# Kernel optimization log

Hardware: AMD Instinct MI355X
Metric: run time of the kernel (lower is better)

## Reference

```python
import jax, jax.numpy as jnp
import numpy as np


def _set_abstraction(xyz, points, npoint, nsample, w1, b1, w2, b2, w3, b3):
    """xyz: (B,3,N), points: (B,C,N) or None. Returns (new_xyz, new_points).
    BN (eval mode) is folded into conv weights/biases; conv1x1 == einsum over channels.
    Deterministic sampling: take first `npoint` points (stand-in for randperm)."""
    B, _, N = xyz.shape
    if npoint is None:
        new_xyz = xyz
        P = N
    else:
        new_xyz = xyz[:, :, :npoint]
        P = npoint
    # squared pairwise distances (B,P,N); topk indices match cdist topk (sqrt monotone)
    xs = jnp.sum(new_xyz * new_xyz, axis=1)            # (B,P)
    ys = jnp.sum(xyz * xyz, axis=1)                    # (B,N)
    d2 = xs[:, :, None] + ys[:, None, :] - 2.0 * jnp.einsum('bcp,bcn->bpn', new_xyz, xyz)
    _, idx = jax.lax.top_k(-d2, nsample)               # (B,P,K) nearest neighbors
    idx4 = idx[:, None, :, :]                          # (B,1,P,K)
    grouped_xyz = jnp.take_along_axis(xyz[:, :, None, :], idx4, axis=3)  # (B,3,P,K)
    grouped_xyz = grouped_xyz - new_xyz[:, :, :, None]
    if points is not None:
        grouped_pts = jnp.take_along_axis(points[:, :, None, :], idx4, axis=3)  # (B,C,P,K)
        feat = jnp.concatenate([grouped_xyz, grouped_pts], axis=1)
    else:
        feat = grouped_xyz
    h = jax.nn.relu(jnp.einsum('oc,bcpk->bopk', w1, feat) + b1[None, :, None, None])
    h = jax.nn.relu(jnp.einsum('oc,bcpk->bopk', w2, h) + b2[None, :, None, None])
    h = jnp.einsum('oc,bcpk->bopk', w3, h) + b3[None, :, None, None]  # no relu before max
    new_points = jnp.max(h, axis=3)                    # (B,C_out,P) max over nsample
    return new_xyz, new_points


def setup_inputs() -> dict:
    key = jax.random.key(0)
    ks = iter(jax.random.split(key, 32))
    B, N, C_IN, NUM_CLASSES = 32, 4096, 6, 40

    def w(k, co, ci):
        return jax.random.normal(k, (co, ci), dtype=jnp.float32) * (1.0 / np.sqrt(ci))

    def b(k, co):
        return jax.random.normal(k, (co,), dtype=jnp.float32) * 0.01

    inp = {'x': jax.random.normal(next(ks), (B, C_IN, N), dtype=jnp.float32)}
    # sa1: in = 3 feat + 3 rel-xyz = 6
    inp['sa1_w1'] = w(next(ks), 64, 6);    inp['sa1_b1'] = b(next(ks), 64)
    inp['sa1_w2'] = w(next(ks), 64, 64);   inp['sa1_b2'] = b(next(ks), 64)
    inp['sa1_w3'] = w(next(ks), 128, 64);  inp['sa1_b3'] = b(next(ks), 128)
    # sa2: in = 128 + 3 = 131
    inp['sa2_w1'] = w(next(ks), 128, 131); inp['sa2_b1'] = b(next(ks), 128)
    inp['sa2_w2'] = w(next(ks), 128, 128); inp['sa2_b2'] = b(next(ks), 128)
    inp['sa2_w3'] = w(next(ks), 256, 128); inp['sa2_b3'] = b(next(ks), 256)
    # sa3: in = 256 + 3 = 259
    inp['sa3_w1'] = w(next(ks), 256, 259); inp['sa3_b1'] = b(next(ks), 256)
    inp['sa3_w2'] = w(next(ks), 512, 256); inp['sa3_b2'] = b(next(ks), 512)
    inp['sa3_w3'] = w(next(ks), 1024, 512); inp['sa3_b3'] = b(next(ks), 1024)
    # fc head (BN folded, dropout in eval mode = identity)
    inp['fc1_w'] = w(next(ks), 512, 1024); inp['fc1_b'] = b(next(ks), 512)
    inp['fc2_w'] = w(next(ks), 256, 512);  inp['fc2_b'] = b(next(ks), 256)
    inp['fc3_w'] = w(next(ks), NUM_CLASSES, 256); inp['fc3_b'] = b(next(ks), NUM_CLASSES)
    return inp


def reference(x, sa1_w1, sa1_b1, sa1_w2, sa1_b2, sa1_w3, sa1_b3,
              sa2_w1, sa2_b1, sa2_w2, sa2_b2, sa2_w3, sa2_b3,
              sa3_w1, sa3_b1, sa3_w2, sa3_b2, sa3_w3, sa3_b3,
              fc1_w, fc1_b, fc2_w, fc2_b, fc3_w, fc3_b):
    xyz = x[:, :3, :]
    pts = x[:, 3:, :]
    xyz1, p1 = _set_abstraction(xyz, pts, 512, 32, sa1_w1, sa1_b1, sa1_w2, sa1_b2, sa1_w3, sa1_b3)
    xyz2, p2 = _set_abstraction(xyz1, p1, 128, 64, sa2_w1, sa2_b1, sa2_w2, sa2_b2, sa2_w3, sa2_b3)
    _, p3 = _set_abstraction(xyz2, p2, None, 1, sa3_w1, sa3_b1, sa3_w2, sa3_b2, sa3_w3, sa3_b3)
    g = jnp.max(p3, axis=2)                               # (B,1024) global max pool
    h = jax.nn.relu(g @ fc1_w.T + fc1_b)                  # dropout eval = identity
    h = jax.nn.relu(h @ fc2_w.T + fc2_b)
    return h @ fc3_w.T + fc3_b                            # (B,num_classes)
```

## Files before the change

kernel.cpp:

```cpp
#include <hip/hip_runtime.h>
#include <hip/hip_bf16.h>

#define FLT_BIG 3.0e38f

typedef __attribute__((ext_vector_type(8))) short s8v;
typedef __attribute__((ext_vector_type(4))) float f4v;

__device__ inline void split3(float v, unsigned short& h0, unsigned short& h1,
                              unsigned short& h2) {
    unsigned int u = __float_as_uint(v);
    h0 = (unsigned short)(u >> 16);
    float r = v - __uint_as_float(u & 0xFFFF0000u);
    unsigned int ru = __float_as_uint(r);
    h1 = (unsigned short)(ru >> 16);
    float r2 = r - __uint_as_float(ru & 0xFFFF0000u);
    h2 = (unsigned short)(__float_as_uint(r2) >> 16);
}

#define SA2_P1(AI, BI)                                                          \
    _Pragma("unroll") for (int oi = 0; oi < 2; oi++) {                          \
        _Pragma("unroll") for (int jf = 0; jf < 4; jf++)                        \
            acc1[oi][jf] = __builtin_amdgcn_mfma_f32_16x16x32_bf16(             \
                aw[oi][AI], bfr[jf][BI], acc1[oi][jf], 0, 0, 0);                \
    }
#define SA1_P1(AI, BI)                                                          \
    _Pragma("unroll") for (int jf = 0; jf < 4; jf++)                            \
        acc1[jf] = __builtin_amdgcn_mfma_f32_16x16x32_bf16(                     \
            aw[AI], bfr[jf][BI], acc1[jf], 0, 0, 0);
#define MM_P2(AI, BI)                                                           \
    _Pragma("unroll") for (int oi = 0; oi < 2; oi++) {                          \
        _Pragma("unroll") for (int jf = 0; jf < 4; jf++)                        \
            acc2[oi][jf] = __builtin_amdgcn_mfma_f32_16x16x32_bf16(             \
                af[jf][AI], gw[oi][BI], acc2[oi][jf], 0, 0, 0);                 \
    }
#define SA3_P(AI, BI)                                                           \
    _Pragma("unroll") for (int oi = 0; oi < 2; oi++) {                          \
        _Pragma("unroll") for (int j = 0; j < 4; j++)                           \
            acc[oi][ph * 4 + j] = __builtin_amdgcn_mfma_f32_16x16x32_bf16(      \
                aw[oi][AI], bfh[j][BI], acc[oi][ph * 4 + j], 0, 0, 0);          \
    }

#define MKKEY(QX, QY, QZ, XS)                                                   \
    ({  float dot_ = fmaf((QZ), yz, fmaf((QY), yy, (QX) * yx));                 \
        float d2_ = fmaf(-2.0f, dot_, (XS) + ys);                               \
        unsigned int kk_ = __float_as_uint(d2_);                                \
        (kk_ & 0x80000000u) ? ~kk_ : (kk_ | 0x80000000u); })

__global__ __launch_bounds__(64) void wfrag_kernel(
    const float* __restrict__ W, int K, int stride, int off, int no,
    unsigned short* __restrict__ out) {
    int bid = blockIdx.x;
    int l = threadIdx.x;
    int ks = bid / no, ot = bid - ks * no;
    int o = ot * 16 + (l & 15);
    int k0 = ks * 32 + (l >> 4) * 8;
    const float* src = W + (size_t)o * stride + off + k0;
    unsigned short h[3][8];
#pragma unroll
    for (int e = 0; e < 8; e++) split3(src[e], h[0][e], h[1][e], h[2][e]);
#pragma unroll
    for (int p = 0; p < 3; p++) {
        s8v v;
#pragma unroll
        for (int e = 0; e < 8; e++) v[e] = (short)h[p][e];
        *(s8v*)(out + ((size_t)(bid * 3 + p) * 64 + l) * 8) = v;
    }
}

__global__ __launch_bounds__(256) void knn4_kernel(
    const float* __restrict__ x, int N_pts, int K, int P, int* __restrict__ idx_out) {
#define KNN_CAP 192
    int bq = blockIdx.x;
    int pg = P >> 2;
    int b = bq / pg, p0 = (bq - b * pg) * 4;
    const float* xyz = x + (size_t)b * 24576;
    __shared__ unsigned int hist[2][2048];
    __shared__ unsigned int candK[4][KNN_CAP];
    __shared__ int candI[4][KNN_CAP];
    __shared__ int outIdx[4][64];
    __shared__ unsigned int cnts[4][2];
    __shared__ int sB[4], sM[4];
    __shared__ float qcoord[4][4];
    int t = threadIdx.x;
    int w = t >> 6, lane = t & 63;
    for (int i = t; i < 4096; i += 256) ((unsigned int*)hist)[i] = 0u;
    if (t < 8) cnts[t >> 1][t & 1] = 0u;
    float qx[4], qy[4], qz[4], xs[4];
#pragma unroll
    for (int q = 0; q < 4; q++) {
        float a = xyz[p0 + q], c1 = xyz[4096 + p0 + q], c2 = xyz[8192 + p0 + q];
        qx[q] = a; qy[q] = c1; qz[q] = c2;
        xs[q] = fmaf(c2, c2, fmaf(c1, c1, a * a));
    }
    if (t < 4) {
        qcoord[t][0] = qx[t]; qcoord[t][1] = qy[t];
        qcoord[t][2] = qz[t]; qcoord[t][3] = xs[t];
    }
    __syncthreads();
    for (int n = t; n < N_pts; n += 256) {
        float yx = xyz[n], yy = xyz[4096 + n], yz = xyz[8192 + n];
        float ys = fmaf(yz, yz, fmaf(yy, yy, yx * yx));
#pragma unroll
        for (int q = 0; q < 4; q++) {
            unsigned int key = MKKEY(qx[q], qy[q], qz[q], xs[q]);
            atomicAdd(&hist[q >> 1][key >> 21], 1u << ((q & 1) * 16));
        }
    }
    __syncthreads();
    {
        int pair = w >> 1, sh = (w & 1) * 16;
        unsigned int lsum = 0;
        for (int i = 0; i < 32; i++)
            lsum += (hist[pair][lane * 32 + i] >> sh) & 0xFFFFu;
        unsigned int incl = lsum;
        for (int s = 1; s < 64; s <<= 1) {
            unsigned int v = (unsigned int)__shfl_up((int)incl, s);
            if (lane >= s) incl += v;
        }
        unsigned int excl = incl - lsum;
        if (excl < (unsigned)K && excl + lsum >= (unsigned)K) {
            unsigned int cum = excl;
            for (int i = 0; i < 32; i++) {
                unsigned int h = (hist[pair][lane * 32 + i] >> sh) & 0xFFFFu;
                if (cum < (unsigned)K && cum + h >= (unsigned)K) {
                    sB[w] = lane * 32 + i; sM[w] = (int)cum; break;
                }
                cum += h;
            }
        }
    }
    __syncthreads();
    for (int n = t; n < N_pts; n += 256) {
        float yx = xyz[n], yy = xyz[4096 + n], yz = xyz[8192 + n];
        float ys = fmaf(yz, yz, fmaf(yy, yy, yx * yx));
#pragma unroll
        for (int q = 0; q < 4; q++) {
            unsigned int key = MKKEY(qx[q], qy[q], qz[q], xs[q]);
            int bin = (int)(key >> 21);
            int Bq = sB[q];
            if (bin < Bq) {
                outIdx[q][atomicAdd(&cnts[q][0], 1u)] = n;
            } else if (bin == Bq) {
                unsigned int ci = atomicAdd(&cnts[q][1], 1u);
                if (ci < KNN_CAP) { candK[q][ci] = key; candI[q][ci] = n; }
            }
        }
    }
    __syncthreads();
    {
        int nc = (int)cnts[w][1];
        int m = sM[w], r = K - m, Bw = sB[w];
        if (nc <= KNN_CAP) {
            for (int ci = lane; ci < nc; ci += 64) {
                unsigned int ki = candK[w][ci];
                int ii = candI[w][ci];
                int rank = 0;
                for (int j = 0; j < nc; j++) {
                    unsigned int kj = candK[w][j];
                    rank += (kj < ki || (kj == ki && candI[w][j] < ii)) ? 1 : 0;
                }
                if (rank < r) outIdx[w][m + rank] = ii;
            }
        } else {
            float fqx = qcoord[w][0], fqy = qcoord[w][1];
            float fqz = qcoord[w][2], fxs = qcoord[w][3];
            unsigned int lastK = 0u; int lastI = -1;
            for (int rr = 0; rr < r; rr++) {
                unsigned int bk = 0xFFFFFFFFu; int bi = 0x7fffffff;
                for (int n = lane; n < N_pts; n += 64) {
                    float yx = xyz[n], yy = xyz[4096 + n], yz = xyz[8192 + n];
                    float ys = fmaf(yz, yz, fmaf(yy, yy, yx * yx));
                    unsigned int key = MKKEY(fqx, fqy, fqz, fxs);
                    if ((int)(key >> 21) == Bw) {
                        bool gt = (key > lastK) || (key == lastK && n > lastI);
                        if (gt && (key < bk || (key == bk && n < bi))) { bk = key; bi = n; }
                    }
                }
#pragma unroll
                for (int s = 32; s > 0; s >>= 1) {
                    unsigned int ok = (unsigned int)__shfl_xor((int)bk, s);
                    int oi = __shfl_xor(bi, s);
                    if (ok < bk || (ok == bk && oi < bi)) { bk = ok; bi = oi; }
                }
                if (lane == 0) outIdx[w][m + rr] = bi;
                lastK = bk; lastI = bi;
            }
        }
    }
    __syncthreads();
    if (t < 4 * K) {
        int q = t / K, k = t - q * K;
        idx_out[((size_t)(b * P) + p0 + q) * K + k] = outIdx[q][k];
    }
}

__global__ __launch_bounds__(256) void sa1_pre_kernel(
    const float* __restrict__ x, const float* __restrict__ w1, const float* __restrict__ b1,
    float* __restrict__ a1t) {
    int bid = blockIdx.x;
    int b = bid >> 5, nt = bid & 31, n0 = nt << 7;
    __shared__ float xsh[6 * 128];
    __shared__ float wt[6 * 68];
    const float* xb = x + (size_t)b * 24576;
    int t = threadIdx.x;
    for (int id = t; id < 768; id += 256) {
        int c = id >> 7, n = id & 127;
        xsh[c * 128 + n] = xb[c * 4096 + n0 + n];
    }
    for (int id = t; id < 384; id += 256) {
        int c = id >> 6, o = id & 63;
        wt[c * 68 + o] = w1[o * 6 + c];
    }
    __syncthreads();
    int o = t & 63, ng = t >> 6;
    float acc[32];
    float bias = b1[o];
#pragma unroll
    for (int j = 0; j < 32; j++) acc[j] = bias;
    for (int c = 0; c < 6; c++) {
        float w = wt[c * 68 + o];
        const float* f = &xsh[c * 128 + ng * 32];
#pragma unroll
        for (int j = 0; j < 32; j++) acc[j] += w * f[j];
    }
#pragma unroll
    for (int j = 0; j < 32; j++)
        a1t[((size_t)b * 4096 + n0 + ng * 32 + j) * 64 + o] = acc[j];
}

__global__ __launch_bounds__(256) void sa1_mfma_kernel(
    const float* __restrict__ x, const float* __restrict__ a1t,
    const int* __restrict__ idx1, const float* __restrict__ w1,
    const unsigned short* __restrict__ w2f, const float* __restrict__ b2,
    const unsigned short* __restrict__ w3f, const float* __restrict__ b3,
    float* __restrict__ p1) {
    int bp = blockIdx.x;
    int b = bp >> 8, pp = bp & 255, p0 = pp * 2;
    __shared__ float dshq[2][64];
    __shared__ int nbr[64];
    __shared__ unsigned short A1buf[8 * 3 * 64 * 8];
    __shared__ float MX[2][128];
    const float* xb = x + (size_t)b * 24576;
    int t = threadIdx.x;
    int w = t >> 6, l = t & 63;
    int n16 = l & 15, og = l >> 4;
    if (t < 64) nbr[t] = idx1[((size_t)b * 512 + p0) * 32 + t];
    if (t < 128) {
        int qi = t >> 6, c = t & 63;
        float qx = xb[p0 + qi], qy = xb[4096 + p0 + qi], qz = xb[8192 + p0 + qi];
        dshq[qi][c] = -(w1[c * 6 + 0] * qx + w1[c * 6 + 1] * qy + w1[c * 6 + 2] * qz);
    }
    __syncthreads();
    int q = w >> 1;
    f4v acc1[4];
#pragma unroll
    for (int jf = 0; jf < 4; jf++) acc1[jf] = (f4v){0.f, 0.f, 0.f, 0.f};
    const float* gsrc = a1t + ((size_t)b * 4096 + nbr[w * 16 + n16]) * 64 + og * 8;
    f4v nv0 = *(const f4v*)(gsrc);
    f4v nv1 = *(const f4v*)(gsrc + 4);
    s8v nw[3];
    {
        const s8v* wr = (const s8v*)w2f;
#pragma unroll
        for (int pl = 0; pl < 3; pl++) nw[pl] = wr[(w * 3 + pl) * 64 + l];
    }
    for (int ks = 0; ks < 2; ks++) {
        f4v v0 = nv0, v1 = nv1;
        s8v aw[3];
#pragma unroll
        for (int pl = 0; pl < 3; pl++) aw[pl] = nw[pl];
        if (ks < 1) {
            nv0 = *(const f4v*)(gsrc + 32);
            nv1 = *(const f4v*)(gsrc + 36);
            const s8v* wr = (const s8v*)w2f + (size_t)4 * 3 * 64;
#pragma unroll
            for (int pl = 0; pl < 3; pl++) nw[pl] = wr[(w * 3 + pl) * 64 + l];
        }
        unsigned short* BFD = A1buf + (ks & 1) * 6144;
        const float* d = &dshq[q][ks * 32 + og * 8];
        s8v sp0, sp1, sp2;
#pragma unroll
        for (int e = 0; e < 8; e++) {
            float hv = fmaxf(((e < 4) ? v0[e] : v1[e - 4]) + d[e], 0.f);
            unsigned short h0, h1, h2;
            split3(hv, h0, h1, h2);
            sp0[e] = (short)h0; sp1[e] = (short)h1; sp2[e] = (short)h2;
        }
        *(s8v*)&BFD[((w * 3 + 0) * 64 + l) * 8] = sp0;
        *(s8v*)&BFD[((w * 3 + 1) * 64 + l) * 8] = sp1;
        *(s8v*)&BFD[((w * 3 + 2) * 64 + l) * 8] = sp2;
        __syncthreads();
        s8v bfr[4][3];
#pragma unroll
        for (int jf = 0; jf < 4; jf++)
#pragma unroll
            for (int pl = 0; pl < 3; pl++)
                bfr[jf][pl] = *(const s8v*)&BFD[((jf * 3 + pl) * 64 + l) * 8];
        SA1_P1(2, 0) SA1_P1(0, 2) SA1_P1(1, 1)
        SA1_P1(1, 0) SA1_P1(0, 1) SA1_P1(0, 0)
    }
    __syncthreads();
    {
        f4v bv = *(const f4v*)(b2 + w * 16 + og * 4);
        int l2 = n16 + ((w & 1) * 2 + (og >> 1)) * 16;
        int half = og & 1;
#pragma unroll
        for (int jf = 0; jf < 4; jf++) {
            unsigned short hh[3][4];
#pragma unroll
            for (int r = 0; r < 4; r++) {
                float y = fmaxf(acc1[jf][r] + bv[r], 0.f);
                split3(y, hh[0][r], hh[1][r], hh[2][r]);
            }
            int slot = (w >> 1) * 4 + jf;
#pragma unroll
            for (int pl = 0; pl < 3; pl++) {
                unsigned long long pk = (unsigned long long)hh[pl][0] |
                    ((unsigned long long)hh[pl][1] << 16) |
                    ((unsigned long long)hh[pl][2] << 32) |
                    ((unsigned long long)hh[pl][3] << 48);
                *(unsigned long long*)&A1buf[((slot * 3 + pl) * 64 + l2) * 8 + half * 4] = pk;
            }
        }
    }
    __syncthreads();
    f4v acc2[2][4];
#pragma unroll
    for (int oi = 0; oi < 2; oi++)
#pragma unroll
        for (int jf = 0; jf < 4; jf++) acc2[oi][jf] = (f4v){0.f, 0.f, 0.f, 0.f};
    for (int ks2 = 0; ks2 < 2; ks2++) {
        s8v af[4][3];
#pragma unroll
        for (int jf = 0; jf < 4; jf++)
#pragma unroll
            for (int pl = 0; pl < 3; pl++)
                af[jf][pl] = *(const s8v*)&A1buf[(((ks2 * 4 + jf) * 3 + pl) * 64 + l) * 8];
        const s8v* wr = (const s8v*)w3f + (size_t)(ks2 * 8) * 3 * 64;
        s8v gw[2][3];
#pragma unroll
        for (int oi = 0; oi < 2; oi++)
#pragma unroll
            for (int pl = 0; pl < 3; pl++)
                gw[oi][pl] = wr[((w * 2 + oi) * 3 + pl) * 64 + l];
        MM_P2(2, 0) MM_P2(0, 2) MM_P2(1, 1)
        MM_P2(1, 0) MM_P2(0, 1) MM_P2(0, 0)
    }
#pragma unroll
    for (int oi = 0; oi < 2; oi++) {
        float m0 = fmaxf(fmaxf(acc2[oi][0][0], acc2[oi][0][1]),
                         fmaxf(acc2[oi][0][2], acc2[oi][0][3]));
        m0 = fmaxf(m0, fmaxf(fmaxf(acc2[oi][1][0], acc2[oi][1][1]),
                             fmaxf(acc2[oi][1][2], acc2[oi][1][3])));
        float m1 = fmaxf(fmaxf(acc2[oi][2][0], acc2[oi][2][1]),
                         fmaxf(acc2[oi][2][2], acc2[oi][2][3]));
        m1 = fmaxf(m1, fmaxf(fmaxf(acc2[oi][3][0], acc2[oi][3][1]),
                             fmaxf(acc2[oi][3][2], acc2[oi][3][3])));
        m0 = fmaxf(m0, __shfl_xor(m0, 16));
        m0 = fmaxf(m0, __shfl_xor(m0, 32));
        m1 = fmaxf(m1, __shfl_xor(m1, 16));
        m1 = fmaxf(m1, __shfl_xor(m1, 32));
        if (og == 0) {
            MX[0][(w * 2 + oi) * 16 + n16] = m0;
            MX[1][(w * 2 + oi) * 16 + n16] = m1;
        }
    }
    __syncthreads();
    {
        int o = t & 127, qq = t >> 7;
        p1[((size_t)b * 128 + o) * 512 + p0 + qq] = MX[qq][o] + b3[o];
    }
}

__global__ __launch_bounds__(256) void sa2_pre_kernel(
    const float* __restrict__ x, const float* __restrict__ p1,
    const float* __restrict__ w1, const float* __restrict__ b1,
    float* __restrict__ a2t) {
    int bid = blockIdx.x;
    int b = bid >> 2, nt = bid & 3, n0 = nt << 7;
    __shared__ float ins[2][16 * 128];
    __shared__ float wt[2][16 * 132];
    const float* xb = x + (size_t)b * 24576;
    const float* p1b = p1 + (size_t)b * 65536;
    int t = threadIdx.x;
    int og = t >> 3, pg = t & 7;
    int o0 = og * 4;
    float acc[4][16];
    {
        float bl[4] = {b1[o0], b1[o0 + 1], b1[o0 + 2], b1[o0 + 3]};
#pragma unroll
        for (int oi = 0; oi < 4; oi++)
#pragma unroll
            for (int j = 0; j < 16; j++) acc[oi][j] = bl[oi];
    }
    for (int id = t; id < 16 * 128; id += 256) {
        int n = id & 127, c = id >> 7;
        ins[0][c * 128 + n] = (c < 3) ? xb[c * 4096 + n0 + n]
                                      : p1b[(size_t)(c - 3) * 512 + n0 + n];
    }
    for (int id = t; id < 2048; id += 256) {
        int c = id & 15, oo = id >> 4;
        wt[0][c * 132 + oo] = w1[oo * 131 + c];
    }
    __syncthreads();
    for (int ch = 0; ch < 9; ch++) {
        int cs = (ch == 8) ? 3 : 16;
        if (ch < 8) {
            int c0n = (ch + 1) * 16;
            int csn = (ch == 7) ? 3 : 16;
            int nb = (ch + 1) & 1;
            for (int id = t; id < csn * 128; id += 256) {
                int n = id & 127, c = id >> 7;
                int cg = c0n + c;
                ins[nb][c * 128 + n] = (cg < 3) ? xb[cg * 4096 + n0 + n]
                                                : p1b[(size_t)(cg - 3) * 512 + n0 + n];
            }
            for (int id = t; id < 2048; id += 256) {
                int c = id & 15, oo = id >> 4;
                if (c < csn) wt[nb][c * 132 + oo] = w1[oo * 131 + c0n + c];
            }
        }
        const float* wb = wt[ch & 1];
        const float* ib = ins[ch & 1];
        for (int cc = 0; cc < cs; cc++) {
            float4 wv = *(const float4*)&wb[cc * 132 + o0];
            float wl[4] = {wv.x, wv.y, wv.z, wv.w};
#pragma unroll
            for (int c4 = 0; c4 < 4; c4++) {
                float4 fv = *(const float4*)&ib[cc * 128 + pg * 4 + c4 * 32];
                float fl[4] = {fv.x, fv.y, fv.z, fv.w};
#pragma unroll
                for (int j = 0; j < 4; j++)
#pragma unroll
                    for (int oi = 0; oi < 4; oi++) acc[oi][c4 * 4 + j] += wl[oi] * fl[j];
            }
        }
        __syncthreads();
    }
#pragma unroll
    for (int c4 = 0; c4 < 4; c4++)
#pragma unroll
        for (int j = 0; j < 4; j++) {
            int n = n0 + pg * 4 + c4 * 32 + j;
            float4 v;
            v.x = acc[0][c4 * 4 + j]; v.y = acc[1][c4 * 4 + j];
            v.z = acc[2][c4 * 4 + j]; v.w = acc[3][c4 * 4 + j];
            *(float4*)&a2t[((size_t)b * 512 + n) * 128 + o0] = v;
        }
}

__global__ __launch_bounds__(256) void sa2_mfma_kernel(
    const float* __restrict__ x, const float* __restrict__ a2t,
    const int* __restrict__ idx2, const float* __restrict__ w1,
    const unsigned short* __restrict__ w2f, const float* __restrict__ b2,
    const unsigned short* __restrict__ w3f, const float* __restrict__ b3,
    unsigned short* __restrict__ p2f) {
    int bp = blockIdx.x;
    int b = bp >> 7, p = bp & 127;
    __shared__ float dsh[128];
    __shared__ int nbr[64];
    __shared__ unsigned short A2buf[16 * 3 * 64 * 8];
    __shared__ float MX[256];
    const float* xb = x + (size_t)b * 24576;
    int t = threadIdx.x;
    int w = t >> 6, l = t & 63;
    int n16 = l & 15, og = l >> 4;
    if (t < 64) nbr[t] = idx2[((size_t)b * 128 + p) * 64 + t];
    if (t < 128) {
        float qx = xb[p], qy = xb[4096 + p], qz = xb[8192 + p];
        dsh[t] = -(w1[t * 131 + 0] * qx + w1[t * 131 + 1] * qy + w1[t * 131 + 2] * qz);
    }
    __syncthreads();
    f4v acc1[2][4];
#pragma unroll
    for (int oi = 0; oi < 2; oi++)
#pragma unroll
        for (int jf = 0; jf < 4; jf++) acc1[oi][jf] = (f4v){0.f, 0.f, 0.f, 0.f};
    const float* gsrc = a2t + ((size_t)b * 512 + nbr[w * 16 + n16]) * 128 + og * 8;
    f4v nv0 = *(const f4v*)(gsrc);
    f4v nv1 = *(const f4v*)(gsrc + 4);
    s8v nw[2][3];
    {
        const s8v* wr = (const s8v*)w2f;
#pragma unroll
        for (int oi = 0; oi < 2; oi++)
#pragma unroll
            for (int pl = 0; pl < 3; pl++)
                nw[oi][pl] = wr[((w * 2 + oi) * 3 + pl) * 64 + l];
    }
    for (int ks = 0; ks < 4; ks++) {
        f4v v0 = nv0, v1 = nv1;
        s8v aw[2][3];
#pragma unroll
        for (int oi = 0; oi < 2; oi++)
#pragma unroll
            for (int pl = 0; pl < 3; pl++) aw[oi][pl] = nw[oi][pl];
        if (ks < 3) {
            nv0 = *(const f4v*)(gsrc + (ks + 1) * 32);
            nv1 = *(const f4v*)(gsrc + (ks + 1) * 32 + 4);
            const s8v* wr = (const s8v*)w2f + (size_t)((ks + 1) * 8) * 3 * 64;
#pragma unroll
            for (int oi = 0; oi < 2; oi++)
#pragma unroll
                for (int pl = 0; pl < 3; pl++)
                    nw[oi][pl] = wr[((w * 2 + oi) * 3 + pl) * 64 + l];
        }
        unsigned short* BFD = A2buf + (ks & 1) * 6144;
        const float* d = &dsh[ks * 32 + og * 8];
        s8v sp0, sp1, sp2;
#pragma unroll
        for (int e = 0; e < 8; e++) {
            float hv = fmaxf(((e < 4) ? v0[e] : v1[e - 4]) + d[e], 0.f);
            unsigned short h0, h1, h2;
            split3(hv, h0, h1, h2);
            sp0[e] = (short)h0; sp1[e] = (short)h1; sp2[e] = (short)h2;
        }
        *(s8v*)&BFD[((w * 3 + 0) * 64 + l) * 8] = sp0;
        *(s8v*)&BFD[((w * 3 + 1) * 64 + l) * 8] = sp1;
        *(s8v*)&BFD[((w * 3 + 2) * 64 + l) * 8] = sp2;
        __syncthreads();
        s8v bfr[4][3];
#pragma unroll
        for (int jf = 0; jf < 4; jf++)
#pragma unroll
            for (int pl = 0; pl < 3; pl++)
                bfr[jf][pl] = *(const s8v*)&BFD[((jf * 3 + pl) * 64 + l) * 8];
        SA2_P1(2, 0) SA2_P1(0, 2) SA2_P1(1, 1)
        SA2_P1(1, 0) SA2_P1(0, 1) SA2_P1(0, 0)
    }
    __syncthreads();
#pragma unroll
    for (int oi = 0; oi < 2; oi++) {
        int ot = w * 2 + oi;
        f4v bv = *(const f4v*)(b2 + ot * 16 + og * 4);
        int l2 = n16 + (oi * 2 + (og >> 1)) * 16;
        int half = og & 1;
#pragma unroll
        for (int jf = 0; jf < 4; jf++) {
            unsigned short hh[3][4];
#pragma unroll
            for (int r = 0; r < 4; r++) {
                float y = fmaxf(acc1[oi][jf][r] + bv[r], 0.f);
                split3(y, hh[0][r], hh[1][r], hh[2][r]);
            }
            int slot = w * 4 + jf;
#pragma unroll
            for (int pl = 0; pl < 3; pl++) {
                unsigned long long pk = (unsigned long long)hh[pl][0] |
                    ((unsigned long long)hh[pl][1] << 16) |
                    ((unsigned long long)hh[pl][2] << 32) |
                    ((unsigned long long)hh[pl][3] << 48);
                *(unsigned long long*)&A2buf[((slot * 3 + pl) * 64 + l2) * 8 + half * 4] = pk;
            }
        }
    }
    __syncthreads();
#pragma unroll
    for (int half2 = 0; half2 < 2; half2++) {
        f4v acc2[2][4];
#pragma unroll
        for (int oi = 0; oi < 2; oi++)
#pragma unroll
            for (int jf = 0; jf < 4; jf++) acc2[oi][jf] = (f4v){0.f, 0.f, 0.f, 0.f};
        for (int ks2 = 0; ks2 < 4; ks2++) {
            s8v af[4][3];
#pragma unroll
            for (int jf = 0; jf < 4; jf++)
#pragma unroll
                for (int pl = 0; pl < 3; pl++)
                    af[jf][pl] = *(const s8v*)&A2buf[(((ks2 * 4 + jf) * 3 + pl) * 64 + l) * 8];
            const s8v* wr = (const s8v*)w3f + (size_t)(ks2 * 16) * 3 * 64;
            s8v gw[2][3];
#pragma unroll
            for (int oi = 0; oi < 2; oi++)
#pragma unroll
                for (int pl = 0; pl < 3; pl++)
                    gw[oi][pl] = wr[((w * 4 + half2 * 2 + oi) * 3 + pl) * 64 + l];
            MM_P2(2, 0) MM_P2(0, 2) MM_P2(1, 1)
            MM_P2(1, 0) MM_P2(0, 1) MM_P2(0, 0)
        }
#pragma unroll
        for (int oi = 0; oi < 2; oi++) {
            float m = -FLT_BIG;
#pragma unroll
            for (int jf = 0; jf < 4; jf++) {
                float mj = fmaxf(fmaxf(acc2[oi][jf][0], acc2[oi][jf][1]),
                                 fmaxf(acc2[oi][jf][2], acc2[oi][jf][3]));
                m = fmaxf(m, mj);
            }
            m = fmaxf(m, __shfl_xor(m, 16));
            m = fmaxf(m, __shfl_xor(m, 32));
            if (og == 0) MX[(w * 4 + half2 * 2 + oi) * 16 + n16] = m;
        }
    }
    __syncthreads();
    {
        float val = MX[t] + b3[t];
        unsigned short h0, h1, h2;
        split3(val, h0, h1, h2);
        int pt = p >> 4;
        int ks = t >> 5, kl = t & 31;
        int l2 = (p & 15) + (kl >> 3) * 16;
        int e = kl & 7;
        size_t fb = (((size_t)b * 64 + ks * 8 + pt) * 3) * 512 + l2 * 8 + e;
        p2f[fb] = h0;
        p2f[fb + 512] = h1;
        p2f[fb + 1024] = h2;
    }
}

__global__ __launch_bounds__(64) void sa3_mfma_kernel(
    const unsigned short* __restrict__ hf_in, const unsigned short* __restrict__ wf,
    const float* __restrict__ bias, int nks, int noCout,
    unsigned short* __restrict__ hf_out, int nksOut,
    float* __restrict__ gout, int reduce) {
    int nb = noCout >> 1;
    int bid = blockIdx.x;
    int b = bid / nb, u = bid - b * nb;
    int ot0 = u * 2;
    int l = threadIdx.x;
    f4v acc[2][8];
#pragma unroll
    for (int oi = 0; oi < 2; oi++)
#pragma unroll
        for (int j = 0; j < 8; j++) acc[oi][j] = (f4v){0.f, 0.f, 0.f, 0.f};
    const unsigned short* hb = hf_in + (size_t)b * nks * 8 * 3 * 512;
    for (int ks = 0; ks < nks; ks++) {
        s8v aw[2][3];
#pragma unroll
        for (int oi = 0; oi < 2; oi++)
#pragma unroll
            for (int pl = 0; pl < 3; pl++)
                aw[oi][pl] = *(const s8v*)&wf[(((size_t)(ks * noCout + ot0 + oi)) * 3 + pl) * 512 + l * 8];
#pragma unroll
        for (int ph = 0; ph < 2; ph++) {
            s8v bfh[4][3];
#pragma unroll
            for (int j = 0; j < 4; j++)
#pragma unroll
                for (int pl = 0; pl < 3; pl++)
                    bfh[j][pl] = *(const s8v*)&hb[(((size_t)(ks * 8 + ph * 4 + j)) * 3 + pl) * 512 + l * 8];
            SA3_P(2, 0) SA3_P(0, 2) SA3_P(1, 1)
            SA3_P(1, 0) SA3_P(0, 1) SA3_P(0, 0)
        }
    }
    if (!reduce) {
#pragma unroll
        for (int oi = 0; oi < 2; oi++) {
            int OT = ot0 + oi;
            f4v bv = *(const f4v*)(bias + OT * 16 + (l >> 4) * 4);
            int ksp = OT >> 1;
            int l2 = (l & 15) + ((OT & 1) * 2 + ((l >> 4) >> 1)) * 16;
            int base4 = ((l >> 4) & 1) * 4;
#pragma unroll
            for (int pt = 0; pt < 8; pt++) {
                unsigned short hh[3][4];
#pragma unroll
                for (int r = 0; r < 4; r++) {
                    float y = fmaxf(acc[oi][pt][r] + bv[r], 0.f);
                    split3(y, hh[0][r], hh[1][r], hh[2][r]);
                }
#pragma unroll
                for (int pl = 0; pl < 3; pl++) {
                    unsigned long long pk = (unsigned long long)hh[pl][0] |
                        ((unsigned long long)hh[pl][1] << 16) |
                        ((unsigned long long)hh[pl][2] << 32) |
                        ((unsigned long long)hh[pl][3] << 48);
                    *(unsigned long long*)&hf_out[
                        (((size_t)b * nksOut * 8 + ksp * 8 + pt) * 3 + pl) * 512 + l2 * 8 + base4] = pk;
                }
            }
        }
    } else {
        int Cout = noCout * 16;
#pragma unroll
        for (int oi = 0; oi < 2; oi++) {
            int OT = ot0 + oi;
#pragma unroll
            for (int r = 0; r < 4; r++) {
                float m = acc[oi][0][r];
#pragma unroll
                for (int pt = 1; pt < 8; pt++) m = fmaxf(m, acc[oi][pt][r]);
                m = fmaxf(m, __shfl_xor(m, 1));
                m = fmaxf(m, __shfl_xor(m, 2));
                m = fmaxf(m, __shfl_xor(m, 4));
                m = fmaxf(m, __shfl_xor(m, 8));
                if ((l & 15) == 0) {
                    int o = OT * 16 + ((l >> 4) << 2) + r;
                    gout[(size_t)b * Cout + o] = m + bias[o];
                }
            }
        }
    }
}

__global__ __launch_bounds__(256) void head1_kernel(
    const float* __restrict__ g, const float* __restrict__ fw1,
    const float* __restrict__ fb1, float* __restrict__ h1out) {
    int bid = blockIdx.x;
    int b = bid >> 3, u = bid & 7;
    int o0 = u * 64;
    __shared__ float gs[1024];
    int t = threadIdx.x;
    for (int i = t; i < 1024; i += 256) gs[i] = g[(size_t)b * 1024 + i];
    __syncthreads();
    int o = o0 + (t >> 2), seg = t & 3;
    const float4* wr = (const float4*)&fw1[(size_t)o * 1024 + seg * 256];
    const float* gg0 = &gs[seg * 256];
    float acc = 0.f;
    for (int c = 0; c < 64; c++) {
        float4 wv = wr[c];
        const float* gg = &gg0[c * 4];
        acc += wv.x * gg[0] + wv.y * gg[1] + wv.z * gg[2] + wv.w * gg[3];
    }
    acc += __shfl_down(acc, 1);
    acc += __shfl_down(acc, 2);
    if (seg == 0) h1out[(size_t)b * 512 + o] = fmaxf(acc + fb1[o], 0.f);
}

__global__ __launch_bounds__(256) void head2_kernel(
    const float* __restrict__ h1in,
    const float* __restrict__ fw2, const float* __restrict__ fb2,
    const float* __restrict__ fw3, const float* __restrict__ fb3,
    float* __restrict__ out) {
    int b = blockIdx.x;
    int t = threadIdx.x;
    __shared__ float h1[512];
    __shared__ float h2[256];
    for (int i = t; i < 512; i += 256) h1[i] = h1in[(size_t)b * 512 + i];
    __syncthreads();
    {
        float acc = fb2[t];
        const float4* wr = (const float4*)&fw2[(size_t)t * 512];
        for (int c = 0; c < 128; c++) {
            float4 wv = wr[c];
            acc += wv.x * h1[c * 4] + wv.y * h1[c * 4 + 1] + wv.z * h1[c * 4 + 2] + wv.w * h1[c * 4 + 3];
        }
        h2[t] = fmaxf(acc, 0.f);
    }
    __syncthreads();
    if (t < 40) {
        float acc = fb3[t];
        const float4* wr = (const float4*)&fw3[(size_t)t * 256];
        for (int c = 0; c < 64; c++) {
            float4 wv = wr[c];
            acc += wv.x * h2[c * 4] + wv.y * h2[c * 4 + 1] + wv.z * h2[c * 4 + 2] + wv.w * h2[c * 4 + 3];
        }
        out[b * 40 + t] = acc;
    }
}

extern "C" void kernel_launch(void* const* d_in, const int* in_sizes, int n_in,
                              void* d_out, int out_size, void* d_ws, size_t ws_size,
                              hipStream_t stream) {
    const float* x      = (const float*)d_in[0];
    const float* sa1_w1 = (const float*)d_in[1];
    const float* sa1_b1 = (const float*)d_in[2];
    const float* sa1_w2 = (const float*)d_in[3];
    const float* sa1_b2 = (const float*)d_in[4];
    const float* sa1_w3 = (const float*)d_in[5];
    const float* sa1_b3 = (const float*)d_in[6];
    const float* sa2_w1 = (const float*)d_in[7];
    const float* sa2_b1 = (const float*)d_in[8];
    const float* sa2_w2 = (const float*)d_in[9];
    const float* sa2_b2 = (const float*)d_in[10];
    const float* sa2_w3 = (const float*)d_in[11];
    const float* sa2_b3 = (const float*)d_in[12];
    const float* sa3_w1 = (const float*)d_in[13];
    const float* sa3_b1 = (const float*)d_in[14];
    const float* sa3_w2 = (const float*)d_in[15];
    const float* sa3_b2 = (const float*)d_in[16];
    const float* sa3_w3 = (const float*)d_in[17];
    const float* sa3_b3 = (const float*)d_in[18];
    const float* fc1_w  = (const float*)d_in[19];
    const float* fc1_b  = (const float*)d_in[20];
    const float* fc2_w  = (const float*)d_in[21];
    const float* fc2_b  = (const float*)d_in[22];
    const float* fc3_w  = (const float*)d_in[23];
    const float* fc3_b  = (const float*)d_in[24];

    char* ws = (char*)d_ws;
    const size_t MB = 1048576;
    const size_t KB = 1024;
    unsigned short* s1w2f = (unsigned short*)(ws + 0);
    unsigned short* s1w3f = (unsigned short*)(ws + 32 * KB);
    unsigned short* s2w2f = (unsigned short*)(ws + 128 * KB);
    unsigned short* s2w3f = (unsigned short*)(ws + 224 * KB);
    int*   idx1 = (int*)  (ws + 512 * KB);
    float* a1t  = (float*)(ws + 3 * MB);
    float* p1   = (float*)(ws + 35 * MB);
    int*   idx2 = (int*)  (ws + 3 * MB);
    float* a2t  = (float*)(ws + 4 * MB);
    unsigned short* p2f = (unsigned short*)(ws + 12 * MB);
    unsigned short* h1f = (unsigned short*)(ws + 18 * MB);
    unsigned short* h2f = (unsigned short*)(ws + 24 * MB);
    float* g     = (float*)(ws + 36 * MB);
    float* h1hd  = (float*)(ws + 36 * MB + 128 * KB);
    unsigned short* w1f3 = (unsigned short*)(ws + 36 * MB + 512 * KB);
    unsigned short* w2f3 = (unsigned short*)(ws + 37 * MB);
    unsigned short* w3f3 = (unsigned short*)(ws + 38 * MB);

    wfrag_kernel<<<2 * 4, 64, 0, stream>>>(sa1_w2, 64, 64, 0, 4, s1w2f);
    wfrag_kernel<<<2 * 8, 64, 0, stream>>>(sa1_w3, 64, 64, 0, 8, s1w3f);
    wfrag_kernel<<<4 * 8, 64, 0, stream>>>(sa2_w2, 128, 128, 0, 8, s2w2f);
    wfrag_kernel<<<4 * 16, 64, 0, stream>>>(sa2_w3, 128, 128, 0, 16, s2w3f);

    knn4_kernel<<<32 * 128, 256, 0, stream>>>(x, 4096, 32, 512, idx1);
    sa1_pre_kernel<<<32 * 32, 256, 0, stream>>>(x, sa1_w1, sa1_b1, a1t);
    sa1_mfma_kernel<<<32 * 256, 256, 0, stream>>>(x, a1t, idx1, sa1_w1,
                                                  s1w2f, sa1_b2, s1w3f, sa1_b3, p1);
    knn4_kernel<<<32 * 32, 256, 0, stream>>>(x, 512, 64, 128, idx2);
    sa2_pre_kernel<<<32 * 4, 256, 0, stream>>>(x, p1, sa2_w1, sa2_b1, a2t);
    wfrag_kernel<<<8 * 16, 64, 0, stream>>>(sa3_w1, 256, 259, 3, 16, w1f3);
    wfrag_kernel<<<8 * 32, 64, 0, stream>>>(sa3_w2, 256, 256, 0, 32, w2f3);
    wfrag_kernel<<<16 * 64, 64, 0, stream>>>(sa3_w3, 512, 512, 0, 64, w3f3);
    sa2_mfma_kernel<<<32 * 128, 256, 0, stream>>>(x, a2t, idx2, sa2_w1,
                                                  s2w2f, sa2_b2, s2w3f, sa2_b3, p2f);
    sa3_mfma_kernel<<<32 * 8, 64, 0, stream>>>(p2f, w1f3, sa3_b1, 8, 16, h1f, 8, nullptr, 0);
    sa3_mfma_kernel<<<32 * 16, 64, 0, stream>>>(h1f, w2f3, sa3_b2, 8, 32, h2f, 16, nullptr, 0);
    sa3_mfma_kernel<<<32 * 32, 64, 0, stream>>>(h2f, w3f3, sa3_b3, 16, 64, nullptr, 0, g, 1);
    head1_kernel<<<32 * 8, 256, 0, stream>>>(g, fc1_w, fc1_b, h1hd);
    head2_kernel<<<32, 256, 0, stream>>>(h1hd, fc2_w, fc2_b, fc3_w, fc3_b,
                                         (float*)d_out);
}
```

Measured before the change: 462.6 us.

## Batch small launches: merge weight-fragment jobs and fuse both KNN passes with SA1 pre

The four SA1/SA2 weight-fragment launches and the three SA3 ones are each merged into a single multi-job kernel. Both KNN passes and the SA1 pre-transform now run in one stage0 kernel that dispatches on block index and shares memory through a union. The second KNN can move earlier because it depends only on x, and its indices are stored as 16-bit. MFMA sections are also wrapped in s_setprio raises, aiming to cut launch gaps and raise overlap at the cost of a larger shared-memory footprint for the pre blocks.

```diff
diff --git a/kernel.cpp b/kernel.cpp
--- a/kernel.cpp
+++ b/kernel.cpp
@@ -46,15 +46,22 @@
         unsigned int kk_ = __float_as_uint(d2_);                                \
         (kk_ & 0x80000000u) ? ~kk_ : (kk_ | 0x80000000u); })
 
-__global__ __launch_bounds__(64) void wfrag_kernel(
-    const float* __restrict__ W, int K, int stride, int off, int no,
-    unsigned short* __restrict__ out) {
+struct WfragJob { const float* W; int K, stride, off, no; unsigned short* out; };
+struct WfragJobs { WfragJob j[4]; int start[5]; };
+
+__global__ __launch_bounds__(64) void wfrag_multi(WfragJobs jobs) {
     int bid = blockIdx.x;
+    int ji = 3;
+    if (bid < jobs.start[1]) ji = 0;
+    else if (bid < jobs.start[2]) ji = 1;
+    else if (bid < jobs.start[3]) ji = 2;
+    const WfragJob& J = jobs.j[ji];
+    int lb = bid - jobs.start[ji];
     int l = threadIdx.x;
-    int ks = bid / no, ot = bid - ks * no;
+    int ks = lb / J.no, ot = lb - ks * J.no;
     int o = ot * 16 + (l & 15);
     int k0 = ks * 32 + (l >> 4) * 8;
-    const float* src = W + (size_t)o * stride + off + k0;
+    const float* src = J.W + (size_t)o * J.stride + J.off + k0;
     unsigned short h[3][8];
 #pragma unroll
     for (int e = 0; e < 8; e++) split3(src[e], h[0][e], h[1][e], h[2][e]);
@@ -63,28 +70,34 @@
         s8v v;
 #pragma unroll
         for (int e = 0; e < 8; e++) v[e] = (short)h[p][e];
-        *(s8v*)(out + ((size_t)(bid * 3 + p) * 64 + l) * 8) = v;
-    }
-}
-
-__global__ __launch_bounds__(256) void knn4_kernel(
-    const float* __restrict__ x, int N_pts, int K, int P, int* __restrict__ idx_out) {
+        *(s8v*)(J.out + ((size_t)(lb * 3 + p) * 64 + l) * 8) = v;
+    }
+}
+
 #define KNN_CAP 192
-    int bq = blockIdx.x;
+struct KnnSmem {
+    unsigned int hist[2][2048];
+    unsigned int candK[4][KNN_CAP];
+    int candI[4][KNN_CAP];
+    int outIdx[4][64];
+    unsigned int cnts[4][2];
+    int sB[4], sM[4];
+    float qcoord[4][4];
+};
+struct Sa1PreSmem { float xsh[6 * 128]; float wt[6 * 68]; };
+union Stage0Smem { KnnSmem knn; Sa1PreSmem pre; };
+
+__device__ void knn4_body(const float* __restrict__ x, int N_pts, int K, int P,
+                          int* __restrict__ idx_out,
+                          unsigned short* __restrict__ idx16,
+                          int bq, KnnSmem& s) {
     int pg = P >> 2;
     int b = bq / pg, p0 = (bq - b * pg) * 4;
     const float* xyz = x + (size_t)b * 24576;
-    __shared__ unsigned int hist[2][2048];
-    __shared__ unsigned int candK[4][KNN_CAP];
-    __shared__ int candI[4][KNN_CAP];
-    __shared__ int outIdx[4][64];
-    __shared__ unsigned int cnts[4][2];
-    __shared__ int sB[4], sM[4];
-    __shared__ float qcoord[4][4];
     int t = threadIdx.x;
     int w = t >> 6, lane = t & 63;
-    for (int i = t; i < 4096; i += 256) ((unsigned int*)hist)[i] = 0u;
-    if (t < 8) cnts[t >> 1][t & 1] = 0u;
+    for (int i = t; i < 4096; i += 256) ((unsigned int*)s.hist)[i] = 0u;
+    if (t < 8) s.cnts[t >> 1][t & 1] = 0u;
     float qx[4], qy[4], qz[4], xs[4];
 #pragma unroll
     for (int q = 0; q < 4; q++) {
@@ -93,8 +106,8 @@
         xs[q] = fmaf(c2, c2, fmaf(c1, c1, a * a));
     }
     if (t < 4) {
-        qcoord[t][0] = qx[t]; qcoord[t][1] = qy[t];
-        qcoord[t][2] = qz[t]; qcoord[t][3] = xs[t];
+        s.qcoord[t][0] = qx[t]; s.qcoord[t][1] = qy[t];
+        s.qcoord[t][2] = qz[t]; s.qcoord[t][3] = xs[t];
     }
     __syncthreads();
     for (int n = t; n < N_pts; n += 256) {
@@ -103,7 +116,7 @@
 #pragma unroll
         for (int q = 0; q < 4; q++) {
             unsigned int key = MKKEY(qx[q], qy[q], qz[q], xs[q]);
-            atomicAdd(&hist[q >> 1][key >> 21], 1u << ((q & 1) * 16));
+            atomicAdd(&s.hist[q >> 1][key >> 21], 1u << ((q & 1) * 16));
         }
     }
     __syncthreads();
@@ -111,19 +124,19 @@
         int pair = w >> 1, sh = (w & 1) * 16;
         unsigned int lsum = 0;
         for (int i = 0; i < 32; i++)
-            lsum += (hist[pair][lane * 32 + i] >> sh) & 0xFFFFu;
+            lsum += (s.hist[pair][lane * 32 + i] >> sh) & 0xFFFFu;
         unsigned int incl = lsum;
-        for (int s = 1; s < 64; s <<= 1) {
-            unsigned int v = (unsigned int)__shfl_up((int)incl, s);
-            if (lane >= s) incl += v;
+        for (int ss = 1; ss < 64; ss <<= 1) {
+            unsigned int v = (unsigned int)__shfl_up((int)incl, ss);
+            if (lane >= ss) incl += v;
         }
         unsigned int excl = incl - lsum;
         if (excl < (unsigned)K && excl + lsum >= (unsigned)K) {
             unsigned int cum = excl;
             for (int i = 0; i < 32; i++) {
-                unsigned int h = (hist[pair][lane * 32 + i] >> sh) & 0xFFFFu;
+                unsigned int h = (s.hist[pair][lane * 32 + i] >> sh) & 0xFFFFu;
                 if (cum < (unsigned)K && cum + h >= (unsigned)K) {
-                    sB[w] = lane * 32 + i; sM[w] = (int)cum; break;
+                    s.sB[w] = lane * 32 + i; s.sM[w] = (int)cum; break;
                 }
                 cum += h;
             }
@@ -137,33 +150,33 @@
         for (int q = 0; q < 4; q++) {
             unsigned int key = MKKEY(qx[q], qy[q], qz[q], xs[q]);
             int bin = (int)(key >> 21);
-            int Bq = sB[q];
+            int Bq = s.sB[q];
             if (bin < Bq) {
-                outIdx[q][atomicAdd(&cnts[q][0], 1u)] = n;
+                s.outIdx[q][atomicAdd(&s.cnts[q][0], 1u)] = n;
             } else if (bin == Bq) {
-                unsigned int ci = atomicAdd(&cnts[q][1], 1u);
-                if (ci < KNN_CAP) { candK[q][ci] = key; candI[q][ci] = n; }
-            }
-        }
-    }
-    __syncthreads();
-    {
-        int nc = (int)cnts[w][1];
-        int m = sM[w], r = K - m, Bw = sB[w];
+                unsigned int ci = atomicAdd(&s.cnts[q][1], 1u);
+                if (ci < KNN_CAP) { s.candK[q][ci] = key; s.candI[q][ci] = n; }
+            }
+        }
+    }
+    __syncthreads();
+    {
+        int nc = (int)s.cnts[w][1];
+        int m = s.sM[w], r = K - m, Bw = s.sB[w];
         if (nc <= KNN_CAP) {
             for (int ci = lane; ci < nc; ci += 64) {
-                unsigned int ki = candK[w][ci];
-                int ii = candI[w][ci];
+                unsigned int ki = s.candK[w][ci];
+                int ii = s.candI[w][ci];
                 int rank = 0;
                 for (int j = 0; j < nc; j++) {
-                    unsigned int kj = candK[w][j];
-                    rank += (kj < ki || (kj == ki && candI[w][j] < ii)) ? 1 : 0;
+                    unsigned int kj = s.candK[w][j];
+                    rank += (kj < ki || (kj == ki && s.candI[w][j] < ii)) ? 1 : 0;
                 }
-                if (rank < r) outIdx[w][m + rank] = ii;
+                if (rank < r) s.outIdx[w][m + rank] = ii;
             }
         } else {
-            float fqx = qcoord[w][0], fqy = qcoord[w][1];
-            float fqz = qcoord[w][2], fxs = qcoord[w][3];
+            float fqx = s.qcoord[w][0], fqy = s.qcoord[w][1];
+            float fqz = s.qcoord[w][2], fxs = s.qcoord[w][3];
             unsigned int lastK = 0u; int lastI = -1;
             for (int rr = 0; rr < r; rr++) {
                 unsigned int bk = 0xFFFFFFFFu; int bi = 0x7fffffff;
@@ -177,12 +190,12 @@
                     }
                 }
 #pragma unroll
-                for (int s = 32; s > 0; s >>= 1) {
-                    unsigned int ok = (unsigned int)__shfl_xor((int)bk, s);
-                    int oi = __shfl_xor(bi, s);
+                for (int ss = 32; ss > 0; ss >>= 1) {
+                    unsigned int ok = (unsigned int)__shfl_xor((int)bk, ss);
+                    int oi = __shfl_xor(bi, ss);
                     if (ok < bk || (ok == bk && oi < bi)) { bk = ok; bi = oi; }
                 }
-                if (lane == 0) outIdx[w][m + rr] = bi;
+                if (lane == 0) s.outIdx[w][m + rr] = bi;
                 lastK = bk; lastI = bi;
             }
         }
@@ -190,26 +203,25 @@
     __syncthreads();
     if (t < 4 * K) {
         int q = t / K, k = t - q * K;
-        idx_out[((size_t)(b * P) + p0 + q) * K + k] = outIdx[q][k];
-    }
-}
-
-__global__ __launch_bounds__(256) void sa1_pre_kernel(
-    const float* __restrict__ x, const float* __restrict__ w1, const float* __restrict__ b1,
-    float* __restrict__ a1t) {
-    int bid = blockIdx.x;
+        size_t off = ((size_t)(b * P) + p0 + q) * K + k;
+        if (idx16) idx16[off] = (unsigned short)s.outIdx[q][k];
+        else idx_out[off] = s.outIdx[q][k];
+    }
+}
+
+__device__ void sa1_pre_body(const float* __restrict__ x, const float* __restrict__ w1,
+                             const float* __restrict__ b1, float* __restrict__ a1t,
+                             int bid, Sa1PreSmem& s) {
     int b = bid >> 5, nt = bid & 31, n0 = nt << 7;
-    __shared__ float xsh[6 * 128];
-    __shared__ float wt[6 * 68];
     const float* xb = x + (size_t)b * 24576;
     int t = threadIdx.x;
     for (int id = t; id < 768; id += 256) {
         int c = id >> 7, n = id & 127;
-        xsh[c * 128 + n] = xb[c * 4096 + n0 + n];
+        s.xsh[c * 128 + n] = xb[c * 4096 + n0 + n];
     }
     for (int id = t; id < 384; id += 256) {
         int c = id >> 6, o = id & 63;
-        wt[c * 68 + o] = w1[o * 6 + c];
+        s.wt[c * 68 + o] = w1[o * 6 + c];
     }
     __syncthreads();
     int o = t & 63, ng = t >> 6;
@@ -218,14 +230,30 @@
 #pragma unroll
     for (int j = 0; j < 32; j++) acc[j] = bias;
     for (int c = 0; c < 6; c++) {
-        float w = wt[c * 68 + o];
-        const float* f = &xsh[c * 128 + ng * 32];
+        float w = s.wt[c * 68 + o];
+        const float* f = &s.xsh[c * 128 + ng * 32];
 #pragma unroll
         for (int j = 0; j < 32; j++) acc[j] += w * f[j];
     }
 #pragma unroll
     for (int j = 0; j < 32; j++)
         a1t[((size_t)b * 4096 + n0 + ng * 32 + j) * 64 + o] = acc[j];
+}
+
+__global__ __launch_bounds__(256) void stage0_kernel(
+    const float* __restrict__ x, int* __restrict__ idx1,
+    unsigned short* __restrict__ idx2_16,
+    const float* __restrict__ w1, const float* __restrict__ b1,
+    float* __restrict__ a1t) {
+    __shared__ Stage0Smem smem;
+    int bid = blockIdx.x;
+    if (bid < 4096) {
+        knn4_body(x, 4096, 32, 512, idx1, nullptr, bid, smem.knn);
+    } else if (bid < 5120) {
+        knn4_body(x, 512, 64, 128, nullptr, idx2_16, bid - 4096, smem.knn);
+    } else {
+        sa1_pre_body(x, w1, b1, a1t, bid - 5120, smem.pre);
+    }
 }
 
 __global__ __launch_bounds__(256) void sa1_mfma_kernel(
@@ -296,8 +324,10 @@
 #pragma unroll
             for (int pl = 0; pl < 3; pl++)
                 bfr[jf][pl] = *(const s8v*)&BFD[((jf * 3 + pl) * 64 + l) * 8];
+        __builtin_amdgcn_s_setprio(1);
         SA1_P1(2, 0) SA1_P1(0, 2) SA1_P1(1, 1)
         SA1_P1(1, 0) SA1_P1(0, 1) SA1_P1(0, 0)
+        __builtin_amdgcn_s_setprio(0);
     }
     __syncthreads();
     {
@@ -343,8 +373,10 @@
 #pragma unroll
             for (int pl = 0; pl < 3; pl++)
                 gw[oi][pl] = wr[((w * 2 + oi) * 3 + pl) * 64 + l];
+        __builtin_amdgcn_s_setprio(1);
         MM_P2(2, 0) MM_P2(0, 2) MM_P2(1, 1)
         MM_P2(1, 0) MM_P2(0, 1) MM_P2(0, 0)
+        __builtin_amdgcn_s_setprio(0);
     }
 #pragma unroll
     for (int oi = 0; oi < 2; oi++) {
@@ -451,7 +483,7 @@
 
 __global__ __launch_bounds__(256) void sa2_mfma_kernel(
     const float* __restrict__ x, const float* __restrict__ a2t,
-    const int* __restrict__ idx2, const float* __restrict__ w1,
+    const unsigned short* __restrict__ idx2, const float* __restrict__ w1,
     const unsigned short* __restrict__ w2f, const float* __restrict__ b2,
     const unsigned short* __restrict__ w3f, const float* __restrict__ b3,
     unsigned short* __restrict__ p2f) {
@@ -465,7 +497,7 @@
     int t = threadIdx.x;
     int w = t >> 6, l = t & 63;
     int n16 = l & 15, og = l >> 4;
-    if (t < 64) nbr[t] = idx2[((size_t)b * 128 + p) * 64 + t];
+    if (t < 64) nbr[t] = (int)idx2[((size_t)b * 128 + p) * 64 + t];
     if (t < 128) {
         float qx = xb[p], qy = xb[4096 + p], qz = xb[8192 + p];
         dsh[t] = -(w1[t * 131 + 0] * qx + w1[t * 131 + 1] * qy + w1[t * 131 + 2] * qz);
@@ -525,8 +557,10 @@
 #pragma unroll
             for (int pl = 0; pl < 3; pl++)
                 bfr[jf][pl] = *(const s8v*)&BFD[((jf * 3 + pl) * 64 + l) * 8];
+        __builtin_amdgcn_s_setprio(1);
         SA2_P1(2, 0) SA2_P1(0, 2) SA2_P1(1, 1)
         SA2_P1(1, 0) SA2_P1(0, 1) SA2_P1(0, 0)
+        __builtin_amdgcn_s_setprio(0);
     }
     __syncthreads();
 #pragma unroll
@@ -576,8 +610,10 @@
 #pragma unroll
                 for (int pl = 0; pl < 3; pl++)
                     gw[oi][pl] = wr[((w * 4 + half2 * 2 + oi) * 3 + pl) * 64 + l];
+            __builtin_amdgcn_s_setprio(1);
             MM_P2(2, 0) MM_P2(0, 2) MM_P2(1, 1)
             MM_P2(1, 0) MM_P2(0, 1) MM_P2(0, 0)
+            __builtin_amdgcn_s_setprio(0);
         }
 #pragma unroll
         for (int oi = 0; oi < 2; oi++) {
@@ -640,8 +676,10 @@
 #pragma unroll
                 for (int pl = 0; pl < 3; pl++)
                     bfh[j][pl] = *(const s8v*)&hb[(((size_t)(ks * 8 + ph * 4 + j)) * 3 + pl) * 512 + l * 8];
+            __builtin_amdgcn_s_setprio(1);
             SA3_P(2, 0) SA3_P(0, 2) SA3_P(1, 1)
             SA3_P(1, 0) SA3_P(0, 1) SA3_P(0, 0)
+            __builtin_amdgcn_s_setprio(0);
         }
     }
     if (!reduce) {
@@ -786,34 +824,44 @@
     unsigned short* s1w3f = (unsigned short*)(ws + 32 * KB);
     unsigned short* s2w2f = (unsigned short*)(ws + 128 * KB);
     unsigned short* s2w3f = (unsigned short*)(ws + 224 * KB);
-    int*   idx1 = (int*)  (ws + 512 * KB);
-    float* a1t  = (float*)(ws + 3 * MB);
-    float* p1   = (float*)(ws + 35 * MB);
-    int*   idx2 = (int*)  (ws + 3 * MB);
-    float* a2t  = (float*)(ws + 4 * MB);
-    unsigned short* p2f = (unsigned short*)(ws + 12 * MB);
-    unsigned short* h1f = (unsigned short*)(ws + 18 * MB);
-    unsigned short* h2f = (unsigned short*)(ws + 24 * MB);
-    float* g     = (float*)(ws + 36 * MB);
-    float* h1hd  = (float*)(ws + 36 * MB + 128 * KB);
-    unsigned short* w1f3 = (unsigned short*)(ws + 36 * MB + 512 * KB);
-    unsigned short* w2f3 = (unsigned short*)(ws + 37 * MB);
-    unsigned short* w3f3 = (unsigned short*)(ws + 38 * MB);
-
-    wfrag_kernel<<<2 * 4, 64, 0, stream>>>(sa1_w2, 64, 64, 0, 4, s1w2f);
-    wfrag_kernel<<<2 * 8, 64, 0, stream>>>(sa1_w3, 64, 64, 0, 8, s1w3f);
-    wfrag_kernel<<<4 * 8, 64, 0, stream>>>(sa2_w2, 128, 128, 0, 8, s2w2f);
-    wfrag_kernel<<<4 * 16, 64, 0, stream>>>(sa2_w3, 128, 128, 0, 16, s2w3f);
-
-    knn4_kernel<<<32 * 128, 256, 0, stream>>>(x, 4096, 32, 512, idx1);
-    sa1_pre_kernel<<<32 * 32, 256, 0, stream>>>(x, sa1_w1, sa1_b1, a1t);
+    int*            idx1  = (int*)(ws + 512 * KB);
+    unsigned short* idx2  = (unsigned short*)(ws + 2560 * KB);
+    float*          a1t   = (float*)(ws + 3 * MB);
+    float*          p1    = (float*)(ws + 35 * MB);
+    float*          a2t   = (float*)(ws + 4 * MB);
+    unsigned short* p2f   = (unsigned short*)(ws + 12 * MB);
+    unsigned short* h1f   = (unsigned short*)(ws + 18 * MB);
+    unsigned short* h2f   = (unsigned short*)(ws + 24 * MB);
+    float*          g     = (float*)(ws + 36 * MB);
+    float*          h1hd  = (float*)(ws + 36 * MB + 128 * KB);
+    unsigned short* w1f3  = (unsigned short*)(ws + 36 * MB + 512 * KB);
+    unsigned short* w2f3  = (unsigned short*)(ws + 37 * MB);
+    unsigned short* w3f3  = (unsigned short*)(ws + 38 * MB);
+
+    {
+        WfragJobs jobs;
+        jobs.j[0] = {sa1_w2, 64, 64, 0, 4, s1w2f};
+        jobs.j[1] = {sa1_w3, 64, 64, 0, 8, s1w3f};
+        jobs.j[2] = {sa2_w2, 128, 128, 0, 8, s2w2f};
+        jobs.j[3] = {sa2_w3, 128, 128, 0, 16, s2w3f};
+        jobs.start[0] = 0; jobs.start[1] = 8; jobs.start[2] = 24;
+        jobs.start[3] = 56; jobs.start[4] = 120;
+        wfrag_multi<<<120, 64, 0, stream>>>(jobs);
+    }
+    stage0_kernel<<<6144, 256, 0, stream>>>(x, idx1, idx2, sa1_w1, sa1_b1, a1t);
     sa1_mfma_kernel<<<32 * 256, 256, 0, stream>>>(x, a1t, idx1, sa1_w1,
                                                   s1w2f, sa1_b2, s1w3f, sa1_b3, p1);
-    knn4_kernel<<<32 * 32, 256, 0, stream>>>(x, 512, 64, 128, idx2);
     sa2_pre_kernel<<<32 * 4, 256, 0, stream>>>(x, p1, sa2_w1, sa2_b1, a2t);
-    wfrag_kernel<<<8 * 16, 64, 0, stream>>>(sa3_w1, 256, 259, 3, 16, w1f3);
-    wfrag_kernel<<<8 * 32, 64, 0, stream>>>(sa3_w2, 256, 256, 0, 32, w2f3);
-    wfrag_kernel<<<16 * 64, 64, 0, stream>>>(sa3_w3, 512, 512, 0, 64, w3f3);
+    {
+        WfragJobs jobs;
+        jobs.j[0] = {sa3_w1, 256, 259, 3, 16, w1f3};
+        jobs.j[1] = {sa3_w2, 256, 256, 0, 32, w2f3};
+        jobs.j[2] = {sa3_w3, 512, 512, 0, 64, w3f3};
+        jobs.j[3] = {sa3_w3, 512, 512, 0, 64, w3f3};
+        jobs.start[0] = 0; jobs.start[1] = 128; jobs.start[2] = 384;
+        jobs.start[3] = 1408; jobs.start[4] = 1408;
+        wfrag_multi<<<1408, 64, 0, stream>>>(jobs);
+    }
     sa2_mfma_kernel<<<32 * 128, 256, 0, stream>>>(x, a2t, idx2, sa2_w1,
                                                   s2w2f, sa2_b2, s2w3f, sa2_b3, p2f);
     sa3_mfma_kernel<<<32 * 8, 64, 0, stream>>>(p2f, w1f3, sa3_b1, 8, 16, h1f, 8, nullptr, 0);
```

New measurement: 498.6 us. 1.08x slower.
